# Kernel optimization log

Measured on AMD Instinct MI355X. Metric: run time of the kernel, lower is better.

Reference implementation:

```python
import jax, jax.numpy as jnp
import numpy as np

# Irreps: in1 = 128x0e + 64x1o + 32x2e, in2 = 16x0e (one-hot-style species attr),
# out = 128x0e + 64x1o + 32x2e.  (mul_in, mul_out, l) per CG path (l x 0e -> l).
PATHS = [(128, 128, 0), (64, 64, 1), (32, 32, 2)]
N_SPECIES = 16
N_NODES = 200_000
DIM_IN = sum(u * (2 * l + 1) for u, _, l in PATHS)   # 480
DIM_OUT = sum(w * (2 * l + 1) for _, w, l in PATHS)  # 480


def setup_inputs() -> dict:
    key = jax.random.key(0)
    k = jax.random.split(key, 5)
    return {
        "x": jax.random.normal(k[0], (N_NODES, DIM_IN), dtype=jnp.float32),
        "operand": jax.random.uniform(k[1], (N_NODES, N_SPECIES), dtype=jnp.float32),
        "w0": jax.random.normal(k[2], (128, N_SPECIES, 128), dtype=jnp.float32),
        "w1": jax.random.normal(k[3], (64, N_SPECIES, 64), dtype=jnp.float32),
        "w2": jax.random.normal(k[4], (32, N_SPECIES, 32), dtype=jnp.float32),
    }


def _path(xl, operand, W, alpha):
    # out[z,w,k] = alpha * sum_{u,v} xl[z,u,k] * operand[z,v] * W[u,v,w]
    # Scan over the small species axis v to avoid a huge [Z,u,w] intermediate.
    Z, u, d = xl.shape
    wm = W.shape[2]

    def step(acc, vin):
        Wv, ov = vin  # Wv: [u, w_out], ov: [Z]
        return acc + ov[:, None, None] * jnp.einsum('zuk,uw->zwk', xl, Wv), None

    init = jnp.zeros((Z, wm, d), dtype=xl.dtype)
    out, _ = jax.lax.scan(step, init, (jnp.moveaxis(W, 1, 0), operand.T))
    return alpha * out


def _fctp(x, operand, weights):
    # e3nn FullyConnectedTensorProduct with in2 = pure 0e scalars:
    # w3j(l, 0, l) = I / sqrt(2l+1); path_weight (component/element norm)
    # = sqrt((2l+1) / (mul_in * n_species))  ->  net alpha = 1/sqrt(mul_in*n_species).
    outs, off = [], 0
    for (u, wm, l), W in zip(PATHS, weights):
        d = 2 * l + 1
        xl = x[:, off:off + u * d].reshape(-1, u, d)  # [Z, mul_in, 2l+1]
        off += u * d
        alpha = jnp.float32(1.0 / float(np.sqrt(u * operand.shape[1])))
        out_l = _path(xl, operand, W, alpha)          # [Z, mul_out, 2l+1]
        outs.append(out_l.reshape(-1, wm * d))
    return jnp.concatenate(outs, axis=-1)             # [Z, 480]


def reference(x, operand, w0, w1, w2):
    return _fctp(x, operand, (w0, w1, w2))
```

## Files before the change

kernel.cpp:

```cpp
#include <hip/hip_runtime.h>
#include <stdint.h>


typedef __attribute__((ext_vector_type(8))) _Float16 f16x8;
typedef __attribute__((ext_vector_type(2))) _Float16 f16x2;
typedef __attribute__((ext_vector_type(4))) float f32x4;

__global__ void prep_wt(const float* __restrict__ w0, const float* __restrict__ w1,
                        const float* __restrict__ w2, unsigned short* __restrict__ wt) {
    int i = blockIdx.x * 256 + threadIdx.x;
    int n, kk, BN, base;
    float v;
    if (i < 262144) {
        base = 0;      n = i >> 11; kk = i & 2047; BN = 128;
        v = w0[kk * 128 + n];
    } else if (i < 327680) {
        int r = i - 262144;
        base = 262144; n = r >> 10; kk = r & 1023; BN = 64;
        v = w1[kk * 64 + n];
    } else {
        int r = i - 327680;
        base = 327680; n = r >> 9;  kk = r & 511;  BN = 32;
        v = w2[kk * 32 + n];
    }
    int t = kk >> 6, c = kk & 63;
    union { _Float16 h; unsigned short s; } u;
    u.h = (_Float16)v;
    wt[base + (t * BN + n) * 64 + (c ^ ((n & 7) * 8))] = u.s;
}

__device__ __forceinline__ void gl_lds16(const void* g, void* l) {
    __builtin_amdgcn_global_load_lds(
        (const __attribute__((address_space(1))) unsigned int*)g,
        (__attribute__((address_space(3))) unsigned int*)l, 16, 0, 0);
}

template<int D, int OFF, int K, int BN, int BM, int WAVES_M, int WAVES_N>
__global__ __launch_bounds__(256, 2)
void fctp_gemm(const float* __restrict__ x, const float* __restrict__ op,
               const unsigned short* __restrict__ wt, float* __restrict__ out,
               int Z, float alpha)
{
    constexpr int BK    = 64;
    constexpr int NSTEP = K / BK;
    constexpr int WTM   = BM / WAVES_M;
    constexpr int WTN   = BN / WAVES_N;
    constexpr int TM    = WTM / 16;
    constexpr int TN    = WTN / 16;
    constexpr int CPW   = BN / 32;
    constexpr int NXL   = (BM == 128) ? 2 : 4;

    __shared__ unsigned short Asm_[2][BM * 64];
    __shared__ unsigned short Bsm_[2][BN * 64];

    const int tid = threadIdx.x;
    const int M   = Z * D;
    const long m0 = (long)blockIdx.x * BM;

    int arow, usel;
    if constexpr (BM == 128) { arow = tid & 127; usel = tid >> 7; }
    else                     { arow = tid;       usel = 0;        }

    long mr = m0 + arow;
    if (mr >= M) mr = M - 1;
    const int zr = (int)(mr / D);
    const int kr = (int)(mr % D);

    f16x2 oh[8];
    #pragma unroll
    for (int j = 0; j < 8; ++j) {
        float a = op[(size_t)zr * 16 + 2 * j];
        float b = op[(size_t)zr * 16 + 2 * j + 1];
        oh[j] = f16x2{(_Float16)a, (_Float16)b};
    }

    const float* xbase = x + (size_t)zr * 480 + OFF + kr;
    if constexpr (BM == 128) xbase += usel * 2 * D;

    const int lane = tid & 63;
    const int wv   = tid >> 6;
    const int wm0  = (wv / WAVES_N) * WTM;
    const int wn0  = (wv % WAVES_N) * WTN;
    const int q    = lane >> 4;
    const int l16  = lane & 15;

    f32x4 acc[TM][TN];
    #pragma unroll
    for (int i = 0; i < TM; ++i)
        #pragma unroll
        for (int j = 0; j < TN; ++j) acc[i][j] = f32x4{0.f, 0.f, 0.f, 0.f};

    float xr[NXL];

    auto xload = [&](int tt) {
        #pragma unroll
        for (int u = 0; u < NXL; ++u) xr[u] = xbase[(size_t)tt * 4 * D + u * D];
    };

    auto buildA = [&](int buf) {
        unsigned short* rowp = &Asm_[buf][arow * 64];
        const int swz = (arow & 7) * 8;
        #pragma unroll
        for (int u = 0; u < NXL; ++u) {
            _Float16 xh = (_Float16)xr[u];
            f16x2 xb2{xh, xh};
            unsigned int pk[8];
            #pragma unroll
            for (int j = 0; j < 8; ++j) {
                f16x2 p = xb2 * oh[j];
                pk[j] = __builtin_bit_cast(unsigned int, p);
            }
            const int cbase = (BM == 128 ? usel * 32 : 0) + u * 16;
            *(uint4*)(rowp + ((cbase    ) ^ swz)) = uint4{pk[0], pk[1], pk[2], pk[3]};
            *(uint4*)(rowp + ((cbase + 8) ^ swz)) = uint4{pk[4], pk[5], pk[6], pk[7]};
        }
    };

    auto dmaB = [&](int buf, int tt) {
        const unsigned short* src = wt + (size_t)tt * BN * 64;
        unsigned short* dst = &Bsm_[buf][0];
        #pragma unroll
        for (int c = 0; c < CPW; ++c) {
            int off = (wv * CPW + c) * 512 + lane * 8;
            gl_lds16(src + off, dst + off);
        }
    };

    auto compute = [&](int buf) {
        #pragma unroll
        for (int h = 0; h < 2; ++h) {
            f16x8 af[TM], bfr[TN];
            #pragma unroll
            for (int i = 0; i < TM; ++i) {
                int row = wm0 + i * 16 + l16;
                af[i] = *(const f16x8*)(&Asm_[buf][row * 64 + ((h * 32 + q * 8) ^ ((row & 7) * 8))]);
            }
            #pragma unroll
            for (int j = 0; j < TN; ++j) {
                int n = wn0 + j * 16 + l16;
                bfr[j] = *(const f16x8*)(&Bsm_[buf][n * 64 + ((h * 32 + q * 8) ^ ((n & 7) * 8))]);
            }
            #pragma unroll
            for (int i = 0; i < TM; ++i)
                #pragma unroll
                for (int j = 0; j < TN; ++j)
                    acc[i][j] = __builtin_amdgcn_mfma_f32_16x16x32_f16(
                        af[i], bfr[j], acc[i][j], 0, 0, 0);
        }
    };

    xload(0);
    dmaB(0, 0);
    buildA(0);
    xload(1);
    __syncthreads();

    for (int t = 0; t < NSTEP; ++t) {
        if (t + 1 < NSTEP) {
            int nb = (t + 1) & 1;
            dmaB(nb, t + 1);
            buildA(nb);
            xload(t + 2 < NSTEP ? t + 2 : NSTEP - 1);
        }
        compute(t & 1);
        if (t + 1 < NSTEP) __syncthreads();
    }

    #pragma unroll
    for (int i = 0; i < TM; ++i) {
        #pragma unroll
        for (int p = 0; p < 4; ++p) {
            long m = m0 + wm0 + i * 16 + q * 4 + p;
            if (m < M) {
                int z = (int)(m / D);
                int k = (int)(m % D);
                float* orow = out + (size_t)z * 480 + OFF + k;
                #pragma unroll
                for (int j = 0; j < TN; ++j) {
                    int col = wn0 + j * 16 + l16;
                    orow[(size_t)col * D] = alpha * acc[i][j][p];
                }
            }
        }
    }
}

extern "C" void kernel_launch(void* const* d_in, const int* in_sizes, int n_in,
                              void* d_out, int out_size, void* d_ws, size_t ws_size,
                              hipStream_t stream) {
    (void)n_in; (void)out_size; (void)ws_size;
    const float* x  = (const float*)d_in[0];
    const float* op = (const float*)d_in[1];
    const float* w0 = (const float*)d_in[2];
    const float* w1 = (const float*)d_in[3];
    const float* w2 = (const float*)d_in[4];
    float* out = (float*)d_out;
    const int Z = in_sizes[0] / 480;

    unsigned short* wt = (unsigned short*)d_ws;
    prep_wt<<<1344, 256, 0, stream>>>(w0, w1, w2, wt);

    const unsigned short* wt0 = wt;
    const unsigned short* wt1 = wt + 262144;
    const unsigned short* wt2 = wt + 327680;

    {
        int M = Z, BM = 128;
        fctp_gemm<1, 0, 2048, 128, 128, 2, 2>
            <<<(M + BM - 1) / BM, 256, 0, stream>>>(x, op, wt0, out, Z, 0.02209708691f);
    }
    {
        int M = Z * 3, BM = 256;
        fctp_gemm<3, 128, 1024, 64, 256, 2, 2>
            <<<(M + BM - 1) / BM, 256, 0, stream>>>(x, op, wt1, out, Z, 0.03125f);
    }
    {
        int M = Z * 5, BM = 256;
        fctp_gemm<5, 320, 512, 32, 256, 4, 1>
            <<<(M + BM - 1) / BM, 256, 0, stream>>>(x, op, wt2, out, Z, 0.04419417382f);
    }
}
```

Baseline: 896.5 us.

## Fuse three path GEMMs into one launch and build A fragments in registers

Merges the three per-irrep GEMM launches into a single kernel that picks the path from the block index, sharing one LDS buffer for the weight tile. The A operand (x times species attributes) is no longer staged through shared memory. Each lane builds its MFMA A fragment directly in registers from prefetched x values. The main loop is unrolled by two with ping-pong register and LDS buffers, and launch bounds rise to 3 blocks per CU. The aim is to remove launch tails, the LDS A traffic and its synchronization, at the cost of more register pressure and redundant x/operand loads across waves.

```diff
diff --git a/kernel.cpp b/kernel.cpp
--- a/kernel.cpp
+++ b/kernel.cpp
@@ -35,54 +35,41 @@
         (__attribute__((address_space(3))) unsigned int*)l, 16, 0, 0);
 }
 
-template<int D, int OFF, int K, int BN, int BM, int WAVES_M, int WAVES_N>
-__global__ __launch_bounds__(256, 2)
-void fctp_gemm(const float* __restrict__ x, const float* __restrict__ op,
-               const unsigned short* __restrict__ wt, float* __restrict__ out,
-               int Z, float alpha)
+template<int D, int OFF, int K, int BN, int BM, int WM, int WN>
+__device__ __forceinline__ void path_run(int bid, const float* __restrict__ x,
+        const float* __restrict__ op, const unsigned short* __restrict__ wt,
+        float* __restrict__ out, int Z, float alpha, unsigned short* Bsm)
 {
-    constexpr int BK    = 64;
-    constexpr int NSTEP = K / BK;
-    constexpr int WTM   = BM / WAVES_M;
-    constexpr int WTN   = BN / WAVES_N;
-    constexpr int TM    = WTM / 16;
-    constexpr int TN    = WTN / 16;
-    constexpr int CPW   = BN / 32;
-    constexpr int NXL   = (BM == 128) ? 2 : 4;
-
-    __shared__ unsigned short Asm_[2][BM * 64];
-    __shared__ unsigned short Bsm_[2][BN * 64];
-
-    const int tid = threadIdx.x;
-    const int M   = Z * D;
-    const long m0 = (long)blockIdx.x * BM;
-
-    int arow, usel;
-    if constexpr (BM == 128) { arow = tid & 127; usel = tid >> 7; }
-    else                     { arow = tid;       usel = 0;        }
-
-    long mr = m0 + arow;
-    if (mr >= M) mr = M - 1;
-    const int zr = (int)(mr / D);
-    const int kr = (int)(mr % D);
-
-    f16x2 oh[8];
+    constexpr int NSTEP = K / 64;
+    constexpr int WTM = BM / WM, WTN = BN / WN;
+    constexpr int TM = WTM / 16, TN = WTN / 16;
+    constexpr int CPW = BN / 32;
+    constexpr int TILE = BN * 64;
+    constexpr int XW = (D == 1) ? 4 : 2;
+
+    const int tid  = threadIdx.x;
+    const int lane = tid & 63, wv = tid >> 6;
+    const int q    = lane >> 4, l16 = lane & 15;
+    const int qh   = q >> 1;
+    const int vh   = (q & 1) * 8;
+    const int wm0  = (wv / WN) * WTM, wn0 = (wv % WN) * WTN;
+    const int M    = Z * D;
+    const long m0  = (long)bid * BM;
+    const char* xb = (const char*)x;
+
+    int xoff[TM];
+    f16x2 oh[TM][4];
     #pragma unroll
-    for (int j = 0; j < 8; ++j) {
-        float a = op[(size_t)zr * 16 + 2 * j];
-        float b = op[(size_t)zr * 16 + 2 * j + 1];
-        oh[j] = f16x2{(_Float16)a, (_Float16)b};
-    }
-
-    const float* xbase = x + (size_t)zr * 480 + OFF + kr;
-    if constexpr (BM == 128) xbase += usel * 2 * D;
-
-    const int lane = tid & 63;
-    const int wv   = tid >> 6;
-    const int wm0  = (wv / WAVES_N) * WTM;
-    const int wn0  = (wv % WAVES_N) * WTN;
-    const int q    = lane >> 4;
-    const int l16  = lane & 15;
+    for (int i = 0; i < TM; ++i) {
+        long m = m0 + wm0 + i * 16 + l16;
+        if (m >= M) m = M - 1;
+        int z = (int)(m / D), kr = (int)(m % D);
+        xoff[i] = z * 1920 + (OFF + kr) * 4 + (D > 1 ? qh * D * 4 : 0);
+        const float* o = op + (size_t)z * 16 + vh;
+        #pragma unroll
+        for (int j2 = 0; j2 < 4; ++j2)
+            oh[i][j2] = f16x2{(_Float16)o[2 * j2], (_Float16)o[2 * j2 + 1]};
+    }
 
     f32x4 acc[TM][TN];
     #pragma unroll
@@ -90,80 +77,112 @@
         #pragma unroll
         for (int j = 0; j < TN; ++j) acc[i][j] = f32x4{0.f, 0.f, 0.f, 0.f};
 
-    float xr[NXL];
-
-    auto xload = [&](int tt) {
-        #pragma unroll
-        for (int u = 0; u < NXL; ++u) xr[u] = xbase[(size_t)tt * 4 * D + u * D];
-    };
-
-    auto buildA = [&](int buf) {
-        unsigned short* rowp = &Asm_[buf][arow * 64];
-        const int swz = (arow & 7) * 8;
-        #pragma unroll
-        for (int u = 0; u < NXL; ++u) {
-            _Float16 xh = (_Float16)xr[u];
-            f16x2 xb2{xh, xh};
-            unsigned int pk[8];
-            #pragma unroll
-            for (int j = 0; j < 8; ++j) {
-                f16x2 p = xb2 * oh[j];
-                pk[j] = __builtin_bit_cast(unsigned int, p);
-            }
-            const int cbase = (BM == 128 ? usel * 32 : 0) + u * 16;
-            *(uint4*)(rowp + ((cbase    ) ^ swz)) = uint4{pk[0], pk[1], pk[2], pk[3]};
-            *(uint4*)(rowp + ((cbase + 8) ^ swz)) = uint4{pk[4], pk[5], pk[6], pk[7]};
-        }
-    };
-
-    auto dmaB = [&](int buf, int tt) {
-        const unsigned short* src = wt + (size_t)tt * BN * 64;
-        unsigned short* dst = &Bsm_[buf][0];
+    float xr0[TM][XW], xr1[TM][XW];
+
+    auto dmaB = [&](int t, int buf) {
+        const unsigned short* src = wt + (size_t)t * TILE;
+        unsigned short* dst = Bsm + buf * TILE;
         #pragma unroll
         for (int c = 0; c < CPW; ++c) {
             int off = (wv * CPW + c) * 512 + lane * 8;
             gl_lds16(src + off, dst + off);
         }
     };
-
-    auto compute = [&](int buf) {
+    auto xloadA = [&](int t) {
+        #pragma unroll
+        for (int i = 0; i < TM; ++i) {
+            if constexpr (D == 1) {
+                f32x4 xv = *(const f32x4*)(xb + xoff[i] + t * 16);
+                xr0[i][0] = xv[0]; xr0[i][1] = xv[1]; xr0[i][2] = xv[2]; xr0[i][3] = xv[3];
+            } else {
+                xr0[i][0] = *(const float*)(xb + xoff[i] + (t * 4    ) * D * 4);
+                xr0[i][1] = *(const float*)(xb + xoff[i] + (t * 4 + 2) * D * 4);
+            }
+        }
+    };
+    auto xloadB = [&](int t) {
+        #pragma unroll
+        for (int i = 0; i < TM; ++i) {
+            if constexpr (D == 1) {
+                f32x4 xv = *(const f32x4*)(xb + xoff[i] + t * 16);
+                xr1[i][0] = xv[0]; xr1[i][1] = xv[1]; xr1[i][2] = xv[2]; xr1[i][3] = xv[3];
+            } else {
+                xr1[i][0] = *(const float*)(xb + xoff[i] + (t * 4    ) * D * 4);
+                xr1[i][1] = *(const float*)(xb + xoff[i] + (t * 4 + 2) * D * 4);
+            }
+        }
+    };
+    auto computeA = [&](int buf) {
+        const unsigned short* bb = Bsm + buf * TILE;
         #pragma unroll
         for (int h = 0; h < 2; ++h) {
-            f16x8 af[TM], bfr[TN];
-            #pragma unroll
-            for (int i = 0; i < TM; ++i) {
-                int row = wm0 + i * 16 + l16;
-                af[i] = *(const f16x8*)(&Asm_[buf][row * 64 + ((h * 32 + q * 8) ^ ((row & 7) * 8))]);
-            }
+            f16x8 bfr[TN];
             #pragma unroll
             for (int j = 0; j < TN; ++j) {
                 int n = wn0 + j * 16 + l16;
-                bfr[j] = *(const f16x8*)(&Bsm_[buf][n * 64 + ((h * 32 + q * 8) ^ ((n & 7) * 8))]);
-            }
-            #pragma unroll
-            for (int i = 0; i < TM; ++i)
+                bfr[j] = *(const f16x8*)(bb + n * 64 + ((h * 32 + q * 8) ^ ((n & 7) * 8)));
+            }
+            #pragma unroll
+            for (int i = 0; i < TM; ++i) {
+                float xs;
+                if constexpr (D == 1) xs = qh ? xr0[i][h * 2 + 1] : xr0[i][h * 2];
+                else                  xs = xr0[i][h];
+                _Float16 xh = (_Float16)xs;
+                f16x2 xx{xh, xh};
+                unsigned int pk[4];
+                #pragma unroll
+                for (int j2 = 0; j2 < 4; ++j2)
+                    pk[j2] = __builtin_bit_cast(unsigned int, xx * oh[i][j2]);
+                f16x8 af = __builtin_bit_cast(f16x8, uint4{pk[0], pk[1], pk[2], pk[3]});
                 #pragma unroll
                 for (int j = 0; j < TN; ++j)
                     acc[i][j] = __builtin_amdgcn_mfma_f32_16x16x32_f16(
-                        af[i], bfr[j], acc[i][j], 0, 0, 0);
-        }
-    };
-
-    xload(0);
+                        af, bfr[j], acc[i][j], 0, 0, 0);
+            }
+        }
+    };
+    auto computeB = [&](int buf) {
+        const unsigned short* bb = Bsm + buf * TILE;
+        #pragma unroll
+        for (int h = 0; h < 2; ++h) {
+            f16x8 bfr[TN];
+            #pragma unroll
+            for (int j = 0; j < TN; ++j) {
+                int n = wn0 + j * 16 + l16;
+                bfr[j] = *(const f16x8*)(bb + n * 64 + ((h * 32 + q * 8) ^ ((n & 7) * 8)));
+            }
+            #pragma unroll
+            for (int i = 0; i < TM; ++i) {
+                float xs;
+                if constexpr (D == 1) xs = qh ? xr1[i][h * 2 + 1] : xr1[i][h * 2];
+                else                  xs = xr1[i][h];
+                _Float16 xh = (_Float16)xs;
+                f16x2 xx{xh, xh};
+                unsigned int pk[4];
+                #pragma unroll
+                for (int j2 = 0; j2 < 4; ++j2)
+                    pk[j2] = __builtin_bit_cast(unsigned int, xx * oh[i][j2]);
+                f16x8 af = __builtin_bit_cast(f16x8, uint4{pk[0], pk[1], pk[2], pk[3]});
+                #pragma unroll
+                for (int j = 0; j < TN; ++j)
+                    acc[i][j] = __builtin_amdgcn_mfma_f32_16x16x32_f16(
+                        af, bfr[j], acc[i][j], 0, 0, 0);
+            }
+        }
+    };
+
     dmaB(0, 0);
-    buildA(0);
-    xload(1);
+    xloadA(0);
     __syncthreads();
 
-    for (int t = 0; t < NSTEP; ++t) {
-        if (t + 1 < NSTEP) {
-            int nb = (t + 1) & 1;
-            dmaB(nb, t + 1);
-            buildA(nb);
-            xload(t + 2 < NSTEP ? t + 2 : NSTEP - 1);
-        }
-        compute(t & 1);
-        if (t + 1 < NSTEP) __syncthreads();
+    for (int t = 0; t < NSTEP; t += 2) {
+        dmaB(t + 1, 1);
+        xloadB(t + 1);
+        computeA(0);
+        __syncthreads();
+        if (t + 2 < NSTEP) { dmaB(t + 2, 0); xloadA(t + 2); }
+        computeB(1);
+        __syncthreads();
     }
 
     #pragma unroll
@@ -172,8 +191,7 @@
         for (int p = 0; p < 4; ++p) {
             long m = m0 + wm0 + i * 16 + q * 4 + p;
             if (m < M) {
-                int z = (int)(m / D);
-                int k = (int)(m % D);
+                int z = (int)(m / D), k = (int)(m % D);
                 float* orow = out + (size_t)z * 480 + OFF + k;
                 #pragma unroll
                 for (int j = 0; j < TN; ++j) {
@@ -183,6 +201,23 @@
             }
         }
     }
+}
+
+__global__ __launch_bounds__(256, 3)
+void fctp_fused(const float* __restrict__ x, const float* __restrict__ op,
+                const unsigned short* __restrict__ wt, float* __restrict__ out,
+                int Z, int nb0, int nb01) {
+    __shared__ unsigned short Bsm[2 * 8192];
+    int bid = blockIdx.x;
+    if (bid < nb0)
+        path_run<1, 0, 2048, 128, 128, 2, 2>(bid, x, op, wt, out, Z,
+                                             0.02209708691f, Bsm);
+    else if (bid < nb01)
+        path_run<3, 128, 1024, 64, 256, 4, 1>(bid - nb0, x, op, wt + 262144, out, Z,
+                                              0.03125f, Bsm);
+    else
+        path_run<5, 320, 512, 32, 256, 4, 1>(bid - nb01, x, op, wt + 327680, out, Z,
+                                             0.04419417382f, Bsm);
 }
 
 extern "C" void kernel_launch(void* const* d_in, const int* in_sizes, int n_in,
@@ -200,23 +235,8 @@
     unsigned short* wt = (unsigned short*)d_ws;
     prep_wt<<<1344, 256, 0, stream>>>(w0, w1, w2, wt);
 
-    const unsigned short* wt0 = wt;
-    const unsigned short* wt1 = wt + 262144;
-    const unsigned short* wt2 = wt + 327680;
-
-    {
-        int M = Z, BM = 128;
-        fctp_gemm<1, 0, 2048, 128, 128, 2, 2>
-            <<<(M + BM - 1) / BM, 256, 0, stream>>>(x, op, wt0, out, Z, 0.02209708691f);
-    }
-    {
-        int M = Z * 3, BM = 256;
-        fctp_gemm<3, 128, 1024, 64, 256, 2, 2>
-            <<<(M + BM - 1) / BM, 256, 0, stream>>>(x, op, wt1, out, Z, 0.03125f);
-    }
-    {
-        int M = Z * 5, BM = 256;
-        fctp_gemm<5, 320, 512, 32, 256, 4, 1>
-            <<<(M + BM - 1) / BM, 256, 0, stream>>>(x, op, wt2, out, Z, 0.04419417382f);
-    }
-}
+    const int nb0 = (Z + 127) / 128;
+    const int nb1 = (3 * Z + 255) / 256;
+    const int nb2 = (5 * Z + 255) / 256;
+    fctp_fused<<<nb0 + nb1 + nb2, 256, 0, stream>>>(x, op, wt, out, Z, nb0, nb0 + nb1);
+}
```

New measurement: 869.0 us. 3.1% less time.
